# Kernel tuning notes

Hardware: AMD Instinct MI355X
Metric: run time of the kernel (lower is better)

The kernel has to match this reference:

```python
import jax, jax.numpy as jnp
import numpy as np

N_LOCS = 100000
N_TIMES = 169
N_USERS = 50000
LOC_DIM = 64
TIME_DIM = 32
USER_DIM = 32
N_HIDDEN = 64
EMB_DIM = LOC_DIM + TIME_DIM + USER_DIM  # 128
OUT_DIM = 2 * N_HIDDEN  # 128
N = 1_000_000


def setup_inputs() -> dict:
    key = jax.random.key(0)
    ks = jax.random.split(key, 8)
    x = jax.random.randint(ks[0], (N, 1), 0, N_LOCS, dtype=jnp.int32)
    t = jax.random.randint(ks[1], (N, 1), 0, N_TIMES, dtype=jnp.int32)
    u = jax.random.randint(ks[2], (N,), 0, N_USERS, dtype=jnp.int32)
    loc_emb = jax.random.normal(ks[3], (N_LOCS, LOC_DIM), jnp.float32) * 0.02
    time_emb = jax.random.normal(ks[4], (N_TIMES, TIME_DIM), jnp.float32) * 0.02
    user_emb = jax.random.normal(ks[5], (N_USERS + 1, USER_DIM), jnp.float32) * 0.02
    user_emb = user_emb.at[0].set(0.0)  # padding_idx=0
    W = jax.random.normal(ks[6], (OUT_DIM, EMB_DIM), jnp.float32) * (1.0 / np.sqrt(EMB_DIM))
    b = jax.random.normal(ks[7], (OUT_DIM,), jnp.float32) * 0.01
    return {"loc_emb": loc_emb, "time_emb": time_emb, "user_emb": user_emb,
            "W": W, "b": b, "x": x, "t": t, "u": u}


def _argunique(x0, t0):
    # hash = t*(x.max()+1) + x, sort, dedupe (padded to N for static shapes)
    n = x0.shape[0]
    h = t0 * (x0.max() + 1) + x0
    idcs = jnp.argsort(h)            # stable sort
    sh = h[idcs]
    mask = jnp.concatenate([jnp.ones((1,), bool), sh[1:] != sh[:-1]])
    group = jnp.cumsum(mask) - 1     # group id per sorted position
    inv = jnp.zeros((n,), jnp.int32).at[idcs].set(group.astype(jnp.int32))
    first_pos = jax.ops.segment_min(jnp.arange(n), group, num_segments=n)
    unique_idcs = idcs[jnp.clip(first_pos, 0, n - 1)]  # rows >= n_unique invalid
    counts = jax.ops.segment_sum(jnp.ones((n,), jnp.float32), group, num_segments=n)
    n_unique = mask.sum()
    return unique_idcs, inv, counts, n_unique


def reference(loc_emb, time_emb, user_emb, W, b, x, t, u):
    n = x.shape[0]
    unique_idcs, inv, counts, n_unique = _argunique(x[:, 0], t[:, 0])
    x_u = x[unique_idcs, 0]
    t_u = t[unique_idcs, 0]
    xt_embed = jnp.concatenate([loc_emb[x_u], time_emb[t_u]], axis=-1)  # [N, 96]
    ui_embed = user_emb[u]                                             # [N, 32]
    u_sum = jax.ops.segment_sum(ui_embed, inv, num_segments=n)         # scatter-add
    u_mean = u_sum / jnp.maximum(counts, 1.0)[:, None]                 # group mean
    xtu = jnp.concatenate([xt_embed, u_mean], axis=-1)                 # [N, 128]
    out = jnp.tanh(xtu @ W.T + b)
    valid = jnp.arange(n)[:, None] < n_unique  # rows past n_unique zeroed (padding)
    return jnp.where(valid, out, 0.0)
```

## Files before the change

### kernel.cpp

```cpp
#include <hip/hip_runtime.h>

#define WORDS    528384
#define NB_SCAN  258

#define IDX_SCALARS 0
#define IDX_MASK1   16
#define IDX_MASK2   (16 + WORDS)
#define IDX_COUNTS  (16 + 2*WORDS)
#define IDX_WBASE(nrows)  (16 + 2*WORDS + (nrows))
#define IDX_PART(nrows)   (IDX_WBASE(nrows) + WORDS)
#define IDX_PART2(nrows)  (IDX_PART(nrows) + 512)
#define IDX_HRANK(nrows)  (IDX_PART2(nrows) + 512)

__device__ __forceinline__ float tanh_fast(float z) {
    float e = __expf(2.0f * z);
    return 1.0f - 2.0f * __builtin_amdgcn_rcpf(e + 1.0f);
}

__global__ void k_init(const int* __restrict__ x, unsigned* __restrict__ scalars,
                       float* __restrict__ out, int n) {
    int g = blockIdx.x * blockDim.x + threadIdx.x;
    int row = g < n ? g : n - 1;
    if (g < n) {
        float4* o4 = (float4*)out + (size_t)row * 32 + 24;
        float4 z = make_float4(0.f, 0.f, 0.f, 0.f);
        #pragma unroll
        for (int q = 0; q < 8; ++q) o4[q] = z;
    }
    unsigned v = (unsigned)x[row];
    #pragma unroll
    for (int off = 32; off > 0; off >>= 1) {
        unsigned o = (unsigned)__shfl_xor((int)v, off);
        v = v > o ? v : o;
    }
    if ((threadIdx.x & 63) == 0) atomicMax(scalars, v);
}

__global__ void k_bits(const int* __restrict__ x, const int* __restrict__ t,
                       const unsigned* __restrict__ scalars,
                       unsigned* __restrict__ mask1, unsigned* __restrict__ mask2, int n) {
    int g = blockIdx.x * blockDim.x + threadIdx.x;
    if (g >= n) return;
    unsigned d = scalars[0] + 1u;
    unsigned h = (unsigned)t[g] * d + (unsigned)x[g];
    unsigned w = h >> 5, bit = 1u << (h & 31);
    unsigned old = atomicOr(&mask1[w], bit);
    if (old & bit) atomicOr(&mask2[w], bit);
}

__global__ void k_scan1(const unsigned* __restrict__ mask1, unsigned* __restrict__ part) {
    const int t = threadIdx.x, b = blockIdx.x;
    const unsigned* wp = mask1 + (size_t)b * 2048 + t * 8;
    unsigned s = 0;
    #pragma unroll
    for (int i = 0; i < 8; ++i) s += __popc(wp[i]);
    #pragma unroll
    for (int off = 32; off > 0; off >>= 1) s += (unsigned)__shfl_xor((int)s, off);
    __shared__ unsigned red[4];
    if ((t & 63) == 0) red[t >> 6] = s;
    __syncthreads();
    if (t == 0) part[b] = red[0] + red[1] + red[2] + red[3];
}

__global__ void k_scan2(const unsigned* __restrict__ part, unsigned* __restrict__ part2,
                        unsigned* __restrict__ scalars) {
    const int t = threadIdx.x;
    __shared__ unsigned sm[512];
    unsigned v = (t < NB_SCAN) ? part[t] : 0u;
    sm[t] = v;
    __syncthreads();
    for (int off = 1; off < 512; off <<= 1) {
        unsigned add = (t >= off) ? sm[t - off] : 0u;
        __syncthreads();
        sm[t] += add;
        __syncthreads();
    }
    part2[t] = sm[t] - v;
    if (t == 511) scalars[1] = sm[511];
}

__global__ void k_scan3(const unsigned* __restrict__ mask1, const unsigned* __restrict__ part2,
                        unsigned* __restrict__ wbase) {
    const int t = threadIdx.x, b = blockIdx.x;
    const int lane = t & 63, wid = t >> 6;
    const size_t w0 = (size_t)b * 2048 + t * 8;
    unsigned pc[8], tsum = 0;
    #pragma unroll
    for (int i = 0; i < 8; ++i) { pc[i] = __popc(mask1[w0 + i]); tsum += pc[i]; }
    unsigned incl = tsum;
    #pragma unroll
    for (int off = 1; off < 64; off <<= 1) {
        unsigned vv = (unsigned)__shfl_up((int)incl, off);
        if (lane >= off) incl += vv;
    }
    __shared__ unsigned wt[4];
    if (lane == 63) wt[wid] = incl;
    __syncthreads();
    unsigned base = part2[b] + (incl - tsum);
    for (int i = 0; i < wid; ++i) base += wt[i];
    #pragma unroll
    for (int i = 0; i < 8; ++i) { wbase[w0 + i] = base; base += pc[i]; }
}

__global__ void k_scatter(const int* __restrict__ x, const int* __restrict__ t,
                          const int* __restrict__ u, const float* __restrict__ user_emb,
                          const unsigned* __restrict__ scalars,
                          const unsigned* __restrict__ mask1, const unsigned* __restrict__ mask2,
                          const unsigned* __restrict__ wbase,
                          unsigned* __restrict__ counts, unsigned* __restrict__ hrank,
                          float* __restrict__ out) {
    int g = blockIdx.x * blockDim.x + threadIdx.x;
    int j = g >> 3, q = g & 7;
    unsigned d = scalars[0] + 1u;
    unsigned h = (unsigned)t[j] * d + (unsigned)x[j];
    unsigned w = h >> 5, bp = h & 31;
    unsigned r = wbase[w] + __popc(mask1[w] & ((1u << bp) - 1u));
    unsigned multi = (mask2[w] >> bp) & 1u;
    float4 ue = ((const float4*)user_emb)[(size_t)u[j] * 8 + q];
    if (multi) {
        float* dst = out + (size_t)r * 128 + 96 + q * 4;
        unsafeAtomicAdd(dst + 0, ue.x);
        unsafeAtomicAdd(dst + 1, ue.y);
        unsafeAtomicAdd(dst + 2, ue.z);
        unsafeAtomicAdd(dst + 3, ue.w);
    } else {
        ((float4*)out)[(size_t)r * 32 + 24 + q] = ue;
    }
    if (q == 0) {
        hrank[r] = h | (multi << 31);
        if (multi) atomicAdd(&counts[r], 1u);
    }
}

__global__ __launch_bounds__(256, 2) void k_gemm(
    const float* __restrict__ loc_emb, const float* __restrict__ time_emb,
    const float* __restrict__ W, const float* __restrict__ bias,
    const unsigned* __restrict__ scalars, const unsigned* __restrict__ counts,
    const unsigned* __restrict__ hrank, float* __restrict__ out, int n) {
    __shared__ float Asm[128 * 64];
    __shared__ float Wsm[128 * 64];
    const int tid = threadIdx.x;
    const unsigned nu = scalars[1];
    const unsigned d  = scalars[0] + 1u;
    const int tx = tid & 15, ty = tid >> 4;
    const int lrow = tid & 63, jj = tid >> 6;
    const int nstripes = (n + 63) >> 6;

    for (int stripe = blockIdx.x; stripe < nstripes; stripe += gridDim.x) {
        {
            unsigned r = (unsigned)stripe * 64u + (unsigned)lrow;
            float4 vals[8];
            if (r < nu) {
                unsigned hv = hrank[r];
                unsigned h = hv & 0x7FFFFFFFu;
                unsigned xx = h % d, tt = h / d;
                if (jj < 2) {
                    const float4* src = (const float4*)(loc_emb + (size_t)xx * 64 + jj * 32);
                    #pragma unroll
                    for (int s = 0; s < 8; ++s) vals[s] = src[s];
                } else if (jj == 2) {
                    const float4* src = (const float4*)(time_emb + (size_t)tt * 32);
                    #pragma unroll
                    for (int s = 0; s < 8; ++s) vals[s] = src[s];
                } else {
                    float inv = (hv >> 31) ? __builtin_amdgcn_rcpf((float)counts[r]) : 1.0f;
                    const float4* src = (const float4*)(out + (size_t)r * 128 + 96);
                    #pragma unroll
                    for (int s = 0; s < 8; ++s) {
                        float4 v = src[s];
                        vals[s] = make_float4(v.x * inv, v.y * inv, v.z * inv, v.w * inv);
                    }
                }
            } else {
                #pragma unroll
                for (int s = 0; s < 8; ++s) vals[s] = make_float4(0.f, 0.f, 0.f, 0.f);
            }
            #pragma unroll
            for (int s = 0; s < 8; ++s) {
                int c = jj * 32 + s * 4;
                Asm[(c + 0) * 64 + lrow] = vals[s].x;
                Asm[(c + 1) * 64 + lrow] = vals[s].y;
                Asm[(c + 2) * 64 + lrow] = vals[s].z;
                Asm[(c + 3) * 64 + lrow] = vals[s].w;
            }
        }
        for (int cb = 0; cb < 2; ++cb) {
            {
                const float* wsrc = W + (size_t)(cb * 64 + lrow) * 128 + jj * 32;
                #pragma unroll
                for (int s = 0; s < 8; ++s) {
                    float4 v = ((const float4*)wsrc)[s];
                    int k0 = jj * 32 + s * 4;
                    Wsm[(k0 + 0) * 64 + lrow] = v.x;
                    Wsm[(k0 + 1) * 64 + lrow] = v.y;
                    Wsm[(k0 + 2) * 64 + lrow] = v.z;
                    Wsm[(k0 + 3) * 64 + lrow] = v.w;
                }
            }
            __syncthreads();
            float acc[4][4];
            #pragma unroll
            for (int i = 0; i < 4; ++i)
                #pragma unroll
                for (int c = 0; c < 4; ++c) acc[i][c] = 0.f;
            #pragma unroll 8
            for (int k = 0; k < 128; ++k) {
                float4 wv = *(const float4*)&Wsm[k * 64 + tx * 4];
                float4 av = *(const float4*)&Asm[k * 64 + ty * 4];
                acc[0][0] += av.x * wv.x; acc[0][1] += av.x * wv.y; acc[0][2] += av.x * wv.z; acc[0][3] += av.x * wv.w;
                acc[1][0] += av.y * wv.x; acc[1][1] += av.y * wv.y; acc[1][2] += av.y * wv.z; acc[1][3] += av.y * wv.w;
                acc[2][0] += av.z * wv.x; acc[2][1] += av.z * wv.y; acc[2][2] += av.z * wv.z; acc[2][3] += av.z * wv.w;
                acc[3][0] += av.w * wv.x; acc[3][1] += av.w * wv.y; acc[3][2] += av.w * wv.z; acc[3][3] += av.w * wv.w;
            }
            float4 bv = ((const float4*)bias)[cb * 16 + tx];
            #pragma unroll
            for (int i = 0; i < 4; ++i) {
                unsigned r = (unsigned)stripe * 64u + (unsigned)(ty * 4 + i);
                if (r >= (unsigned)n) continue;
                float4 o;
                if (r < nu) {
                    o.x = tanh_fast(acc[i][0] + bv.x);
                    o.y = tanh_fast(acc[i][1] + bv.y);
                    o.z = tanh_fast(acc[i][2] + bv.z);
                    o.w = tanh_fast(acc[i][3] + bv.w);
                } else {
                    o = make_float4(0.f, 0.f, 0.f, 0.f);
                }
                ((float4*)(out + (size_t)r * 128 + cb * 64))[tx] = o;
            }
            __syncthreads();
        }
    }
}

extern "C" void kernel_launch(void* const* d_in, const int* in_sizes, int n_in,
                              void* d_out, int out_size, void* d_ws, size_t ws_size,
                              hipStream_t stream) {
    const float* loc_emb  = (const float*)d_in[0];
    const float* time_emb = (const float*)d_in[1];
    const float* user_emb = (const float*)d_in[2];
    const float* W        = (const float*)d_in[3];
    const float* bias     = (const float*)d_in[4];
    const int*   x        = (const int*)d_in[5];
    const int*   t        = (const int*)d_in[6];
    const int*   u        = (const int*)d_in[7];
    float* out = (float*)d_out;
    const int n = in_sizes[5];

    unsigned* ws32    = (unsigned*)d_ws;
    unsigned* scalars = ws32 + IDX_SCALARS;
    unsigned* mask1   = ws32 + IDX_MASK1;
    unsigned* mask2   = ws32 + IDX_MASK2;
    unsigned* counts  = ws32 + IDX_COUNTS;
    unsigned* wbase   = ws32 + IDX_WBASE(n);
    unsigned* part    = ws32 + IDX_PART(n);
    unsigned* part2   = ws32 + IDX_PART2(n);
    unsigned* hrank   = ws32 + IDX_HRANK(n);

    const size_t zero_bytes = (size_t)(16 + 2 * WORDS + n) * 4;
    hipMemsetAsync(d_ws, 0, zero_bytes, stream);

    int nb = (n + 255) / 256;
    k_init   <<<nb, 256, 0, stream>>>(x, scalars, out, n);
    k_bits   <<<nb, 256, 0, stream>>>(x, t, scalars, mask1, mask2, n);
    k_scan1  <<<NB_SCAN, 256, 0, stream>>>(mask1, part);
    k_scan2  <<<1, 512, 0, stream>>>(part, part2, scalars);
    k_scan3  <<<NB_SCAN, 256, 0, stream>>>(mask1, part2, wbase);
    k_scatter<<<n / 32, 256, 0, stream>>>(x, t, u, user_emb, scalars, mask1, mask2,
                                          wbase, counts, hrank, out);
    k_gemm   <<<1024, 256, 0, stream>>>(loc_emb, time_emb, W, bias, scalars, counts,
                                        hrank, out, n);
}
```

Measured before the change: 1.237 ms.

## Use split-bf16 MFMA for projection and skip user-embedding staging for singleton rows

The FP32 LDS-tiled GEMM is replaced with MFMA 16x16x32 bf16 instructions using a hi/lo split, three products per tile, to approximate FP32 accuracy. W stays in registers for the whole kernel, so no shared memory is used. Singleton groups now store their user index in counts so the GEMM reads user_emb directly, and only multi-occurrence rows are zeroed and atomically accumulated. Stripes fully past n_unique just write zeros. The split-bf16 path carries some accuracy risk, and the packed x/t encoding assumes x fits in 17 bits and t in 8 bits.

```diff
diff --git a/kernel.cpp b/kernel.cpp
--- a/kernel.cpp
+++ b/kernel.cpp
@@ -12,21 +12,31 @@
 #define IDX_PART2(nrows)  (IDX_PART(nrows) + 512)
 #define IDX_HRANK(nrows)  (IDX_PART2(nrows) + 512)
 
+typedef __attribute__((ext_vector_type(8))) short s8x;
+typedef __attribute__((ext_vector_type(4))) float f4x;
+
 __device__ __forceinline__ float tanh_fast(float z) {
     float e = __expf(2.0f * z);
     return 1.0f - 2.0f * __builtin_amdgcn_rcpf(e + 1.0f);
 }
 
-__global__ void k_init(const int* __restrict__ x, unsigned* __restrict__ scalars,
-                       float* __restrict__ out, int n) {
+__device__ __forceinline__ unsigned bfr(float f) {
+    unsigned u = __float_as_uint(f);
+    return (u + 0x7FFFu + ((u >> 16) & 1u)) >> 16;
+}
+
+__device__ __forceinline__ void split8(const float* fv, s8x& hi, s8x& lo) {
+    #pragma unroll
+    for (int e = 0; e < 8; ++e) {
+        unsigned hb = bfr(fv[e]);
+        hi[e] = (short)hb;
+        lo[e] = (short)bfr(fv[e] - __uint_as_float(hb << 16));
+    }
+}
+
+__global__ void k_init(const int* __restrict__ x, unsigned* __restrict__ scalars, int n) {
     int g = blockIdx.x * blockDim.x + threadIdx.x;
     int row = g < n ? g : n - 1;
-    if (g < n) {
-        float4* o4 = (float4*)out + (size_t)row * 32 + 24;
-        float4 z = make_float4(0.f, 0.f, 0.f, 0.f);
-        #pragma unroll
-        for (int q = 0; q < 8; ++q) o4[q] = z;
-    }
     unsigned v = (unsigned)x[row];
     #pragma unroll
     for (int off = 32; off > 0; off >>= 1) {
@@ -102,133 +112,180 @@
     for (int i = 0; i < 8; ++i) { wbase[w0 + i] = base; base += pc[i]; }
 }
 
+__global__ void k_zero_multi(const unsigned* __restrict__ mask1, const unsigned* __restrict__ mask2,
+                             const unsigned* __restrict__ wbase, float* __restrict__ out) {
+    int w = blockIdx.x * blockDim.x + threadIdx.x;
+    if (w >= WORDS) return;
+    unsigned m2 = mask2[w];
+    if (!m2) return;
+    unsigned m1 = mask1[w];
+    unsigned base = wbase[w];
+    float4 z = make_float4(0.f, 0.f, 0.f, 0.f);
+    do {
+        int b = __builtin_ctz(m2);
+        m2 &= m2 - 1u;
+        unsigned r = base + __popc(m1 & ((1u << b) - 1u));
+        float4* dst = (float4*)(out + (size_t)r * 128 + 96);
+        #pragma unroll
+        for (int q = 0; q < 8; ++q) dst[q] = z;
+    } while (m2);
+}
+
 __global__ void k_scatter(const int* __restrict__ x, const int* __restrict__ t,
                           const int* __restrict__ u, const float* __restrict__ user_emb,
                           const unsigned* __restrict__ scalars,
                           const unsigned* __restrict__ mask1, const unsigned* __restrict__ mask2,
                           const unsigned* __restrict__ wbase,
                           unsigned* __restrict__ counts, unsigned* __restrict__ hrank,
-                          float* __restrict__ out) {
-    int g = blockIdx.x * blockDim.x + threadIdx.x;
-    int j = g >> 3, q = g & 7;
-    unsigned d = scalars[0] + 1u;
-    unsigned h = (unsigned)t[j] * d + (unsigned)x[j];
+                          float* __restrict__ out, int n) {
+    int j = blockIdx.x * blockDim.x + threadIdx.x;
+    if (j >= n) return;
+    unsigned d  = scalars[0] + 1u;
+    unsigned xv = (unsigned)x[j], tv = (unsigned)t[j];
+    unsigned h = tv * d + xv;
     unsigned w = h >> 5, bp = h & 31;
     unsigned r = wbase[w] + __popc(mask1[w] & ((1u << bp) - 1u));
     unsigned multi = (mask2[w] >> bp) & 1u;
-    float4 ue = ((const float4*)user_emb)[(size_t)u[j] * 8 + q];
-    if (multi) {
-        float* dst = out + (size_t)r * 128 + 96 + q * 4;
-        unsafeAtomicAdd(dst + 0, ue.x);
-        unsafeAtomicAdd(dst + 1, ue.y);
-        unsafeAtomicAdd(dst + 2, ue.z);
-        unsafeAtomicAdd(dst + 3, ue.w);
+    unsigned pack = xv | (tv << 17) | (multi << 31);
+    hrank[r] = pack;
+    if (!multi) {
+        counts[r] = (unsigned)u[j];
     } else {
-        ((float4*)out)[(size_t)r * 32 + 24 + q] = ue;
-    }
-    if (q == 0) {
-        hrank[r] = h | (multi << 31);
-        if (multi) atomicAdd(&counts[r], 1u);
+        atomicAdd(&counts[r], 1u);
+        const float4* ue = (const float4*)(user_emb + (size_t)u[j] * 32);
+        float* dst = out + (size_t)r * 128 + 96;
+        #pragma unroll
+        for (int q = 0; q < 8; ++q) {
+            float4 v = ue[q];
+            unsafeAtomicAdd(dst + q * 4 + 0, v.x);
+            unsafeAtomicAdd(dst + q * 4 + 1, v.y);
+            unsafeAtomicAdd(dst + q * 4 + 2, v.z);
+            unsafeAtomicAdd(dst + q * 4 + 3, v.w);
+        }
     }
 }
 
 __global__ __launch_bounds__(256, 2) void k_gemm(
     const float* __restrict__ loc_emb, const float* __restrict__ time_emb,
+    const float* __restrict__ user_emb,
     const float* __restrict__ W, const float* __restrict__ bias,
     const unsigned* __restrict__ scalars, const unsigned* __restrict__ counts,
     const unsigned* __restrict__ hrank, float* __restrict__ out, int n) {
-    __shared__ float Asm[128 * 64];
-    __shared__ float Wsm[128 * 64];
-    const int tid = threadIdx.x;
+    const int tid  = threadIdx.x;
+    const int wave = tid >> 6, lane = tid & 63;
+    const int lr = lane & 15, lg = lane >> 4;
+    const int wrow = wave & 1, wcol = wave >> 1;
+    const int cbase = wcol * 64;
     const unsigned nu = scalars[1];
-    const unsigned d  = scalars[0] + 1u;
-    const int tx = tid & 15, ty = tid >> 4;
-    const int lrow = tid & 63, jj = tid >> 6;
+
+    s8x bhi[4][4], blo[4][4];
+    {
+        const float* wr = W + (size_t)(cbase + lr) * 128 + lg * 8;
+        #pragma unroll
+        for (int ct = 0; ct < 4; ++ct) {
+            #pragma unroll
+            for (int ks = 0; ks < 4; ++ks) {
+                const float4* p = (const float4*)(wr + ct * 16 * 128 + ks * 32);
+                float4 v0 = p[0], v1 = p[1];
+                float fv[8] = {v0.x, v0.y, v0.z, v0.w, v1.x, v1.y, v1.z, v1.w};
+                split8(fv, bhi[ct][ks], blo[ct][ks]);
+            }
+        }
+    }
+    float bv[4];
+    #pragma unroll
+    for (int ct = 0; ct < 4; ++ct) bv[ct] = bias[cbase + ct * 16 + lr];
+
     const int nstripes = (n + 63) >> 6;
-
     for (int stripe = blockIdx.x; stripe < nstripes; stripe += gridDim.x) {
+        const int r0 = stripe * 64;
+        if ((unsigned)r0 >= nu) {
+            int rows = (n - r0 < 64) ? (n - r0) : 64;
+            float4 z = make_float4(0.f, 0.f, 0.f, 0.f);
+            float4* o4 = (float4*)(out + (size_t)r0 * 128);
+            for (int i = tid; i < rows * 32; i += 256) o4[i] = z;
+            continue;
+        }
+        const int rb = r0 + wrow * 32;
+
+        unsigned xx[2], tt[2], cnt[2], mlt[2];
+        bool val[2];
+        #pragma unroll
+        for (int rt = 0; rt < 2; ++rt) {
+            unsigned r = (unsigned)(rb + rt * 16 + lr);
+            val[rt] = r < nu;
+            unsigned hv = val[rt] ? hrank[r] : 0u;
+            xx[rt]  = hv & 0x1FFFFu;
+            tt[rt]  = (hv >> 17) & 0xFFu;
+            mlt[rt] = hv >> 31;
+            cnt[rt] = val[rt] ? counts[r] : 0u;
+        }
+
+        f4x acc[2][4];
         {
-            unsigned r = (unsigned)stripe * 64u + (unsigned)lrow;
-            float4 vals[8];
-            if (r < nu) {
-                unsigned hv = hrank[r];
-                unsigned h = hv & 0x7FFFFFFFu;
-                unsigned xx = h % d, tt = h / d;
-                if (jj < 2) {
-                    const float4* src = (const float4*)(loc_emb + (size_t)xx * 64 + jj * 32);
-                    #pragma unroll
-                    for (int s = 0; s < 8; ++s) vals[s] = src[s];
-                } else if (jj == 2) {
-                    const float4* src = (const float4*)(time_emb + (size_t)tt * 32);
-                    #pragma unroll
-                    for (int s = 0; s < 8; ++s) vals[s] = src[s];
+            f4x z = {0.f, 0.f, 0.f, 0.f};
+            #pragma unroll
+            for (int rt = 0; rt < 2; ++rt)
+                #pragma unroll
+                for (int ct = 0; ct < 4; ++ct) acc[rt][ct] = z;
+        }
+
+        #pragma unroll
+        for (int ks = 0; ks < 4; ++ks) {
+            s8x ahi[2], alo[2];
+            #pragma unroll
+            for (int rt = 0; rt < 2; ++rt) {
+                if (val[rt]) {
+                    const float4* p;
+                    float sc = 1.0f;
+                    if (ks == 0)      p = (const float4*)(loc_emb  + (size_t)xx[rt] * 64 + lg * 8);
+                    else if (ks == 1) p = (const float4*)(loc_emb  + (size_t)xx[rt] * 64 + 32 + lg * 8);
+                    else if (ks == 2) p = (const float4*)(time_emb + (size_t)tt[rt] * 32 + lg * 8);
+                    else {
+                        if (mlt[rt]) {
+                            p  = (const float4*)(out + (size_t)(rb + rt * 16 + lr) * 128 + 96 + lg * 8);
+                            sc = __builtin_amdgcn_rcpf((float)cnt[rt]);
+                        } else {
+                            p  = (const float4*)(user_emb + (size_t)cnt[rt] * 32 + lg * 8);
+                        }
+                    }
+                    float4 v0 = p[0], v1 = p[1];
+                    float fv[8] = {v0.x * sc, v0.y * sc, v0.z * sc, v0.w * sc,
+                                   v1.x * sc, v1.y * sc, v1.z * sc, v1.w * sc};
+                    split8(fv, ahi[rt], alo[rt]);
                 } else {
-                    float inv = (hv >> 31) ? __builtin_amdgcn_rcpf((float)counts[r]) : 1.0f;
-                    const float4* src = (const float4*)(out + (size_t)r * 128 + 96);
-                    #pragma unroll
-                    for (int s = 0; s < 8; ++s) {
-                        float4 v = src[s];
-                        vals[s] = make_float4(v.x * inv, v.y * inv, v.z * inv, v.w * inv);
-                    }
-                }
-            } else {
-                #pragma unroll
-                for (int s = 0; s < 8; ++s) vals[s] = make_float4(0.f, 0.f, 0.f, 0.f);
-            }
-            #pragma unroll
-            for (int s = 0; s < 8; ++s) {
-                int c = jj * 32 + s * 4;
-                Asm[(c + 0) * 64 + lrow] = vals[s].x;
-                Asm[(c + 1) * 64 + lrow] = vals[s].y;
-                Asm[(c + 2) * 64 + lrow] = vals[s].z;
-                Asm[(c + 3) * 64 + lrow] = vals[s].w;
-            }
-        }
-        for (int cb = 0; cb < 2; ++cb) {
-            {
-                const float* wsrc = W + (size_t)(cb * 64 + lrow) * 128 + jj * 32;
-                #pragma unroll
-                for (int s = 0; s < 8; ++s) {
-                    float4 v = ((const float4*)wsrc)[s];
-                    int k0 = jj * 32 + s * 4;
-                    Wsm[(k0 + 0) * 64 + lrow] = v.x;
-                    Wsm[(k0 + 1) * 64 + lrow] = v.y;
-                    Wsm[(k0 + 2) * 64 + lrow] = v.z;
-                    Wsm[(k0 + 3) * 64 + lrow] = v.w;
+                    s8x z = {0, 0, 0, 0, 0, 0, 0, 0};
+                    ahi[rt] = z; alo[rt] = z;
                 }
             }
-            __syncthreads();
-            float acc[4][4];
-            #pragma unroll
-            for (int i = 0; i < 4; ++i)
+            #pragma unroll
+            for (int ct = 0; ct < 4; ++ct) {
                 #pragma unroll
-                for (int c = 0; c < 4; ++c) acc[i][c] = 0.f;
-            #pragma unroll 8
-            for (int k = 0; k < 128; ++k) {
-                float4 wv = *(const float4*)&Wsm[k * 64 + tx * 4];
-                float4 av = *(const float4*)&Asm[k * 64 + ty * 4];
-                acc[0][0] += av.x * wv.x; acc[0][1] += av.x * wv.y; acc[0][2] += av.x * wv.z; acc[0][3] += av.x * wv.w;
-                acc[1][0] += av.y * wv.x; acc[1][1] += av.y * wv.y; acc[1][2] += av.y * wv.z; acc[1][3] += av.y * wv.w;
-                acc[2][0] += av.z * wv.x; acc[2][1] += av.z * wv.y; acc[2][2] += av.z * wv.z; acc[2][3] += av.z * wv.w;
-                acc[3][0] += av.w * wv.x; acc[3][1] += av.w * wv.y; acc[3][2] += av.w * wv.z; acc[3][3] += av.w * wv.w;
+                for (int rt = 0; rt < 2; ++rt) {
+                    f4x c = acc[rt][ct];
+                    c = __builtin_amdgcn_mfma_f32_16x16x32_bf16(ahi[rt], bhi[ct][ks], c, 0, 0, 0);
+                    c = __builtin_amdgcn_mfma_f32_16x16x32_bf16(alo[rt], bhi[ct][ks], c, 0, 0, 0);
+                    c = __builtin_amdgcn_mfma_f32_16x16x32_bf16(ahi[rt], blo[ct][ks], c, 0, 0, 0);
+                    acc[rt][ct] = c;
+                }
             }
-            float4 bv = ((const float4*)bias)[cb * 16 + tx];
-            #pragma unroll
-            for (int i = 0; i < 4; ++i) {
-                unsigned r = (unsigned)stripe * 64u + (unsigned)(ty * 4 + i);
-                if (r >= (unsigned)n) continue;
-                float4 o;
-                if (r < nu) {
-                    o.x = tanh_fast(acc[i][0] + bv.x);
-                    o.y = tanh_fast(acc[i][1] + bv.y);
-                    o.z = tanh_fast(acc[i][2] + bv.z);
-                    o.w = tanh_fast(acc[i][3] + bv.w);
-                } else {
-                    o = make_float4(0.f, 0.f, 0.f, 0.f);
+        }
+
+        __syncthreads();
+
+        #pragma unroll
+        for (int rt = 0; rt < 2; ++rt) {
+            #pragma unroll
+            for (int ct = 0; ct < 4; ++ct) {
+                const int c = cbase + ct * 16 + lr;
+                #pragma unroll
+                for (int p = 0; p < 4; ++p) {
+                    int rr = rb + rt * 16 + lg * 4 + p;
+                    float o = 0.f;
+                    if ((unsigned)rr < nu) o = tanh_fast(acc[rt][ct][p] + bv[ct]);
+                    if (rr < n) out[(size_t)rr * 128 + c] = o;
                 }
-                ((float4*)(out + (size_t)r * 128 + cb * 64))[tx] = o;
             }
-            __syncthreads();
         }
     }
 }
@@ -261,13 +318,14 @@
     hipMemsetAsync(d_ws, 0, zero_bytes, stream);
 
     int nb = (n + 255) / 256;
-    k_init   <<<nb, 256, 0, stream>>>(x, scalars, out, n);
-    k_bits   <<<nb, 256, 0, stream>>>(x, t, scalars, mask1, mask2, n);
-    k_scan1  <<<NB_SCAN, 256, 0, stream>>>(mask1, part);
-    k_scan2  <<<1, 512, 0, stream>>>(part, part2, scalars);
-    k_scan3  <<<NB_SCAN, 256, 0, stream>>>(mask1, part2, wbase);
-    k_scatter<<<n / 32, 256, 0, stream>>>(x, t, u, user_emb, scalars, mask1, mask2,
-                                          wbase, counts, hrank, out);
-    k_gemm   <<<1024, 256, 0, stream>>>(loc_emb, time_emb, W, bias, scalars, counts,
-                                        hrank, out, n);
-}
+    k_init      <<<nb, 256, 0, stream>>>(x, scalars, n);
+    k_bits      <<<nb, 256, 0, stream>>>(x, t, scalars, mask1, mask2, n);
+    k_scan1     <<<NB_SCAN, 256, 0, stream>>>(mask1, part);
+    k_scan2     <<<1, 512, 0, stream>>>(part, part2, scalars);
+    k_scan3     <<<NB_SCAN, 256, 0, stream>>>(mask1, part2, wbase);
+    k_zero_multi<<<(WORDS + 255) / 256, 256, 0, stream>>>(mask1, mask2, wbase, out);
+    k_scatter   <<<nb, 256, 0, stream>>>(x, t, u, user_emb, scalars, mask1, mask2,
+                                         wbase, counts, hrank, out, n);
+    k_gemm      <<<3125, 256, 0, stream>>>(loc_emb, time_emb, user_emb, W, bias,
+                                           scalars, counts, hrank, out, n);
+}
```

Measured after the change: 1.115 ms. 1.11x faster.
